# Optimization experiments

Measured on AMD Instinct MI355X. Metric: run time of the kernel, lower is better.

Reference implementation:

```python
import jax, jax.numpy as jnp
import numpy as np

IN_FEATURES = 4096
OUT_FEATURES = 4096


def setup_inputs() -> dict:
    key = jax.random.key(0)
    k_x, k_w, k_b = jax.random.split(key, 3)
    inp = {
        "input": jax.random.normal(k_x, (4, 2048, IN_FEATURES), dtype=jnp.float32),
        # learned int8 weight table [out_features, in_features]
        "weight_int8": jax.random.randint(k_w, (OUT_FEATURES, IN_FEATURES), -128, 128, dtype=jnp.int32).astype(jnp.int8),
        # per-tensor dequant scales (scalars, as in the module buffers)
        "scale": jnp.asarray(0.01, dtype=jnp.float32),
        "x_scale": jnp.asarray(0.05, dtype=jnp.float32),
        "bias": jax.random.normal(k_b, (OUT_FEATURES,), dtype=jnp.float32) * 0.02,
    }
    return inp


def reference(input, weight_int8, scale, x_scale, bias):
    # --- quantize activations per-tensor to int8 (W8A8 path) ---
    x_int8 = jnp.clip(jnp.round(input / x_scale), -128, 127).astype(jnp.int8)
    in_shape = input.shape
    x_flat = x_int8.reshape(-1, in_shape[-1])  # [B*S, in]
    # contract x_flat[k] with weight_int8[n, k] -> [B*S, out]
    out_i32 = jax.lax.dot_general(
        x_flat, weight_int8,
        dimension_numbers=(((1,), (1,)), ((), ())),
        preferred_element_type=jnp.int32,
    )
    # --- dequant epilogue: combined scale, reshape, bias ---
    out = out_i32.astype(input.dtype) * (scale * x_scale)
    out = out.reshape(*in_shape[:-1], weight_int8.shape[0])
    out = out + bias
    return out
```

## Files before the change

### kernel.cpp

```cpp
#include <hip/hip_runtime.h>

#define KDIM 4096
#define NDIM 4096
#define BM 128
#define BN 256
#define BK 64
#define NTILE (KDIM / BK)
#define BUFSZ 24576
#define NBUF 3

using i32x4 = __attribute__((ext_vector_type(4))) int;

__device__ __forceinline__ void g2l16(const void* g, void* l) {
  __builtin_amdgcn_global_load_lds(
      (const __attribute__((address_space(1))) void*)g,
      (__attribute__((address_space(3))) void*)l,
      16, 0, 0);
}

__global__ void w8l_detect(const int* __restrict__ w32, int* __restrict__ flag) {
  __shared__ int s;
  const int t = threadIdx.x;
  if (t == 0) s = 1;
  __syncthreads();
  bool oob = false;
#pragma unroll
  for (int i = 0; i < 16; ++i) {
    int v = w32[t * 16 + i];
    if (v < -128 || v > 127) oob = true;
  }
  if (oob) atomicAnd(&s, 0);
  __syncthreads();
  if (t == 0) *flag = s;
}

__global__ void w8l_pack(const void* __restrict__ wsrc, const int* __restrict__ flag,
                         signed char* __restrict__ wq) {
  if (*flag == 0) return;
  const int t = blockIdx.x * blockDim.x + threadIdx.x;
  const int4* s = (const int4*)wsrc;
  int4 a = s[t * 4 + 0], b = s[t * 4 + 1], c = s[t * 4 + 2], d = s[t * 4 + 3];
  int4 o;
  o.x = (a.x & 255) | ((a.y & 255) << 8) | ((a.z & 255) << 16) | ((a.w & 255) << 24);
  o.y = (b.x & 255) | ((b.y & 255) << 8) | ((b.z & 255) << 16) | ((b.w & 255) << 24);
  o.z = (c.x & 255) | ((c.y & 255) << 8) | ((c.z & 255) << 16) | ((c.w & 255) << 24);
  o.w = (d.x & 255) | ((d.y & 255) << 8) | ((d.z & 255) << 16) | ((d.w & 255) << 24);
  ((int4*)wq)[t] = o;
}

__global__ void w8l_quant(const float* __restrict__ x, const float* __restrict__ xs,
                          signed char* __restrict__ xq) {
  const int t = blockIdx.x * blockDim.x + threadIdx.x;
  const float s = *xs;
  const float4* x4 = (const float4*)x;
  int4 o;
  int* op = (int*)&o;
#pragma unroll
  for (int q = 0; q < 4; ++q) {
    float4 f = x4[t * 4 + q];
    int v0 = __float2int_rn(f.x / s);
    int v1 = __float2int_rn(f.y / s);
    int v2 = __float2int_rn(f.z / s);
    int v3 = __float2int_rn(f.w / s);
    v0 = v0 < -128 ? -128 : (v0 > 127 ? 127 : v0);
    v1 = v1 < -128 ? -128 : (v1 > 127 ? 127 : v1);
    v2 = v2 < -128 ? -128 : (v2 > 127 ? 127 : v2);
    v3 = v3 < -128 ? -128 : (v3 > 127 ? 127 : v3);
    op[q] = (v0 & 255) | ((v1 & 255) << 8) | ((v2 & 255) << 16) | ((v3 & 255) << 24);
  }
  ((int4*)xq)[t] = o;
}

__global__ __launch_bounds__(256, 2) void w8l_gemm(
    const signed char* __restrict__ Aq,
    const signed char* __restrict__ Wraw, const signed char* __restrict__ Wpk,
    const int* __restrict__ flag,
    const float* __restrict__ scale, const float* __restrict__ xscale,
    const float* __restrict__ bias, float* __restrict__ out, int nbn) {
  __shared__ signed char lds[NBUF * BUFSZ];

  const signed char* __restrict__ Wq = (*flag) ? Wpk : Wraw;

  const int tid = threadIdx.x;
  const int lane = tid & 63;
  const int wid = tid >> 6;
  const int wr = wid >> 1;
  const int wc = wid & 1;
  const int l15 = lane & 15;
  const int l4 = (lane >> 4) & 3;

  const int nwg = gridDim.x;
  const int cpx = nwg >> 3;
  const int bid = blockIdx.x;
  const int swz = (bid & 7) * cpx + (bid >> 3);
  const int bm = swz / nbn, bn = swz % nbn;
  const int m0 = bm * BM, n0 = bn * BN;

  const unsigned r_in = (unsigned)tid >> 2;
  const unsigned c16 = (unsigned)tid & 3;
  const unsigned s_in = (r_in >> 1) & 3u;
  const unsigned swcol = ((c16 ^ s_in) << 4);
  const signed char* agp = Aq + (size_t)(m0 + r_in) * KDIM + swcol;
  const signed char* wgp = Wq + (size_t)(n0 + r_in) * KDIM + swcol;
  const unsigned ldsoff = (unsigned)tid * 16u;

#define ISSUE_TILE(t, buf)                                                   \
  do {                                                                       \
    const size_t koff_ = (size_t)(t) * BK;                                   \
    signed char* lb_ = lds + (unsigned)(buf) * BUFSZ + ldsoff;               \
    _Pragma("unroll") for (int u = 0; u < 2; ++u)                            \
      g2l16(agp + (size_t)(u * 64) * KDIM + koff_, lb_ + u * 4096);          \
    _Pragma("unroll") for (int u = 0; u < 4; ++u)                            \
      g2l16(wgp + (size_t)(u * 64) * KDIM + koff_, lb_ + 8192 + u * 4096);   \
  } while (0)

  const unsigned slotoff = (unsigned)((l4 ^ ((l15 >> 1) & 3)) << 4);
  const unsigned arow = (unsigned)((wr * 64 + l15) * 64) + slotoff;
  const unsigned brow = (unsigned)((wc * 128 + l15) * 64) + slotoff + 8192u;

  i32x4 acc[4][8] = {};
  i32x4 af[4], bf[8];

  ISSUE_TILE(0, 0);
  ISSUE_TILE(1, 1);

  int bufr = 0, bufi = 2;
#pragma unroll 1
  for (int kt = 0; kt < NTILE; ++kt) {
    if (kt + 2 < NTILE) {
      asm volatile("s_waitcnt vmcnt(6)" ::: "memory");
    } else {
      asm volatile("s_waitcnt vmcnt(0)" ::: "memory");
    }
    __builtin_amdgcn_s_barrier();
    __builtin_amdgcn_sched_barrier(0);

    if (kt + 2 < NTILE) ISSUE_TILE(kt + 2, bufi);

    const signed char* base = lds + (unsigned)bufr * BUFSZ;
#pragma unroll
    for (int mi = 0; mi < 4; ++mi)
      af[mi] = *(const i32x4*)(base + arow + mi * 1024);
#pragma unroll
    for (int nj = 0; nj < 8; ++nj)
      bf[nj] = *(const i32x4*)(base + brow + nj * 1024);
    __builtin_amdgcn_sched_barrier(0);
    asm volatile("s_waitcnt lgkmcnt(0)" ::: "memory");
    __builtin_amdgcn_sched_barrier(0);

    __builtin_amdgcn_s_setprio(1);
#pragma unroll
    for (int mi = 0; mi < 4; ++mi)
#pragma unroll
      for (int nj = 0; nj < 8; ++nj)
        acc[mi][nj] = __builtin_amdgcn_mfma_i32_16x16x64_i8(af[mi], bf[nj], acc[mi][nj], 0, 0, 0);
    __builtin_amdgcn_s_setprio(0);
    __builtin_amdgcn_sched_barrier(0);

    bufr = (bufr == 2) ? 0 : bufr + 1;
    bufi = (bufi == 2) ? 0 : bufi + 1;
  }

  const float cs = scale[0] * xscale[0];
#pragma unroll
  for (int nj = 0; nj < 8; ++nj) {
    const int n = n0 + wc * 128 + nj * 16 + l15;
    const float bj = bias[n];
#pragma unroll
    for (int mi = 0; mi < 4; ++mi) {
      const int m = m0 + wr * 64 + mi * 16 + l4 * 4;
      float* o = out + (size_t)m * NDIM + n;
#pragma unroll
      for (int v = 0; v < 4; ++v)
        o[(size_t)v * NDIM] = (float)acc[mi][nj][v] * cs + bj;
    }
  }
#undef ISSUE_TILE
}

extern "C" void kernel_launch(void* const* d_in, const int* in_sizes, int n_in,
                              void* d_out, int out_size, void* d_ws, size_t ws_size,
                              hipStream_t stream) {
  const float* x = (const float*)d_in[0];
  const void* w = d_in[1];
  const float* scale = (const float*)d_in[2];
  const float* xscale = (const float*)d_in[3];
  const float* bias = (const float*)d_in[4];
  float* out = (float*)d_out;

  const int M = in_sizes[0] / KDIM;

  int* flag = (int*)d_ws;
  signed char* wq = (signed char*)d_ws + 256;
  signed char* aq = wq + (size_t)NDIM * KDIM;

  const size_t need = 256 + (size_t)NDIM * KDIM + (size_t)M * KDIM;
  if (ws_size < need) return;

  w8l_detect<<<1, 256, 0, stream>>>((const int*)w, flag);
  w8l_pack<<<(NDIM * KDIM / 16) / 256, 256, 0, stream>>>(w, flag, wq);
  w8l_quant<<<(M * KDIM / 16) / 256, 256, 0, stream>>>(x, xscale, aq);

  const int nbn = NDIM / BN;
  w8l_gemm<<<(M / BM) * nbn, 256, 0, stream>>>(
      aq, (const signed char*)w, wq, flag, scale, xscale, bias, out, nbn);
}
```

Measured before the change: 198.2 us.

## Load A fragments directly to registers and split MFMA phase on LDS waits

The A operand no longer goes through LDS. Each wave reads its A fragments straight from global memory into registers, double-buffered one tile ahead. Only B is staged through LDS, which shrinks the LDS footprint, and the main loop is unrolled by two so the register buffers can alternate. The MFMA block is also split in half around a partial lgkmcnt wait, letting compute start before all B reads finish. The cost is more global traffic for A, since the two waves sharing rows each load them, plus higher register pressure and vmcnt accounting that must be exactly right.

```diff
diff --git a/kernel.cpp b/kernel.cpp
--- a/kernel.cpp
+++ b/kernel.cpp
@@ -6,7 +6,7 @@
 #define BN 256
 #define BK 64
 #define NTILE (KDIM / BK)
-#define BUFSZ 24576
+#define BBUF 16384
 #define NBUF 3
 
 using i32x4 = __attribute__((ext_vector_type(4))) int;
@@ -77,7 +77,7 @@
     const int* __restrict__ flag,
     const float* __restrict__ scale, const float* __restrict__ xscale,
     const float* __restrict__ bias, float* __restrict__ out, int nbn) {
-  __shared__ signed char lds[NBUF * BUFSZ];
+  __shared__ signed char lds[NBUF * BBUF];
 
   const signed char* __restrict__ Wq = (*flag) ? Wpk : Wraw;
 
@@ -98,68 +98,88 @@
 
   const unsigned r_in = (unsigned)tid >> 2;
   const unsigned c16 = (unsigned)tid & 3;
-  const unsigned s_in = (r_in >> 1) & 3u;
-  const unsigned swcol = ((c16 ^ s_in) << 4);
-  const signed char* agp = Aq + (size_t)(m0 + r_in) * KDIM + swcol;
+  const unsigned swcol = ((c16 ^ ((r_in >> 1) & 3u)) << 4);
   const signed char* wgp = Wq + (size_t)(n0 + r_in) * KDIM + swcol;
   const unsigned ldsoff = (unsigned)tid * 16u;
 
-#define ISSUE_TILE(t, buf)                                                   \
+#define ISSUE_B(t, buf)                                                      \
   do {                                                                       \
     const size_t koff_ = (size_t)(t) * BK;                                   \
-    signed char* lb_ = lds + (unsigned)(buf) * BUFSZ + ldsoff;               \
-    _Pragma("unroll") for (int u = 0; u < 2; ++u)                            \
-      g2l16(agp + (size_t)(u * 64) * KDIM + koff_, lb_ + u * 4096);          \
+    signed char* lb_ = lds + (unsigned)(buf) * BBUF + ldsoff;                \
     _Pragma("unroll") for (int u = 0; u < 4; ++u)                            \
-      g2l16(wgp + (size_t)(u * 64) * KDIM + koff_, lb_ + 8192 + u * 4096);   \
+      g2l16(wgp + (size_t)(u * 64) * KDIM + koff_, lb_ + u * 4096);          \
   } while (0)
 
+  const signed char* agl = Aq + (size_t)(m0 + wr * 64 + l15) * KDIM + l4 * 16;
+
+#define LOAD_A(dst, t)                                                       \
+  _Pragma("unroll") for (int mi = 0; mi < 4; ++mi)                           \
+      dst[mi] = *(const i32x4*)(agl + (size_t)mi * (16 * KDIM) + (t) * 64);
+
   const unsigned slotoff = (unsigned)((l4 ^ ((l15 >> 1) & 3)) << 4);
-  const unsigned arow = (unsigned)((wr * 64 + l15) * 64) + slotoff;
-  const unsigned brow = (unsigned)((wc * 128 + l15) * 64) + slotoff + 8192u;
+  const unsigned brow = (unsigned)((wc * 128 + l15) * 64) + slotoff;
 
   i32x4 acc[4][8] = {};
-  i32x4 af[4], bf[8];
-
-  ISSUE_TILE(0, 0);
-  ISSUE_TILE(1, 1);
+  i32x4 aE[4], aO[4], bf[8];
+
+#define SB __builtin_amdgcn_sched_barrier(0)
+
+#define TILE(t, AC, AN, DO_A, DO_G, bufr_, bufi_, VMC)                       \
+  do {                                                                       \
+    asm volatile("s_waitcnt vmcnt(" #VMC ")" ::: "memory");                  \
+    __builtin_amdgcn_s_barrier();                                            \
+    SB;                                                                      \
+    if (DO_A) { LOAD_A(AN, (t) + 1); }                                       \
+    SB;                                                                      \
+    if (DO_G) ISSUE_B((t) + 2, bufi_);                                       \
+    SB;                                                                      \
+    {                                                                        \
+      const signed char* base_ = lds + (unsigned)(bufr_)*BBUF;               \
+      _Pragma("unroll") for (int nj = 0; nj < 8; ++nj)                       \
+          bf[nj] = *(const i32x4*)(base_ + brow + nj * 1024);                \
+    }                                                                        \
+    SB;                                                                      \
+    asm volatile("s_waitcnt lgkmcnt(4)" ::: "memory");                       \
+    SB;                                                                      \
+    __builtin_amdgcn_s_setprio(1);                                           \
+    _Pragma("unroll") for (int mi = 0; mi < 4; ++mi)                         \
+        _Pragma("unroll") for (int nj = 0; nj < 4; ++nj)                     \
+            acc[mi][nj] = __builtin_amdgcn_mfma_i32_16x16x64_i8(             \
+                AC[mi], bf[nj], acc[mi][nj], 0, 0, 0);                       \
+    __builtin_amdgcn_s_setprio(0);                                           \
+    SB;                                                                      \
+    asm volatile("s_waitcnt lgkmcnt(0)" ::: "memory");                       \
+    SB;                                                                      \
+    __builtin_amdgcn_s_setprio(1);                                           \
+    _Pragma("unroll") for (int mi = 0; mi < 4; ++mi)                         \
+        _Pragma("unroll") for (int nj = 4; nj < 8; ++nj)                     \
+            acc[mi][nj] = __builtin_amdgcn_mfma_i32_16x16x64_i8(             \
+                AC[mi], bf[nj], acc[mi][nj], 0, 0, 0);                       \
+    __builtin_amdgcn_s_setprio(0);                                           \
+    SB;                                                                      \
+  } while (0)
+
+  ISSUE_B(0, 0);
+  SB;
+  LOAD_A(aE, 0);
+  SB;
+  ISSUE_B(1, 1);
+  SB;
 
   int bufr = 0, bufi = 2;
 #pragma unroll 1
-  for (int kt = 0; kt < NTILE; ++kt) {
-    if (kt + 2 < NTILE) {
-      asm volatile("s_waitcnt vmcnt(6)" ::: "memory");
-    } else {
-      asm volatile("s_waitcnt vmcnt(0)" ::: "memory");
-    }
-    __builtin_amdgcn_s_barrier();
-    __builtin_amdgcn_sched_barrier(0);
-
-    if (kt + 2 < NTILE) ISSUE_TILE(kt + 2, bufi);
-
-    const signed char* base = lds + (unsigned)bufr * BUFSZ;
-#pragma unroll
-    for (int mi = 0; mi < 4; ++mi)
-      af[mi] = *(const i32x4*)(base + arow + mi * 1024);
-#pragma unroll
-    for (int nj = 0; nj < 8; ++nj)
-      bf[nj] = *(const i32x4*)(base + brow + nj * 1024);
-    __builtin_amdgcn_sched_barrier(0);
-    asm volatile("s_waitcnt lgkmcnt(0)" ::: "memory");
-    __builtin_amdgcn_sched_barrier(0);
-
-    __builtin_amdgcn_s_setprio(1);
-#pragma unroll
-    for (int mi = 0; mi < 4; ++mi)
-#pragma unroll
-      for (int nj = 0; nj < 8; ++nj)
-        acc[mi][nj] = __builtin_amdgcn_mfma_i32_16x16x64_i8(af[mi], bf[nj], acc[mi][nj], 0, 0, 0);
-    __builtin_amdgcn_s_setprio(0);
-    __builtin_amdgcn_sched_barrier(0);
-
+  for (int t2 = 0; t2 < NTILE - 2; t2 += 2) {
+    TILE(t2, aE, aO, 1, 1, bufr, bufi, 4);
     bufr = (bufr == 2) ? 0 : bufr + 1;
     bufi = (bufi == 2) ? 0 : bufi + 1;
-  }
+    TILE(t2 + 1, aO, aE, 1, 1, bufr, bufi, 4);
+    bufr = (bufr == 2) ? 0 : bufr + 1;
+    bufi = (bufi == 2) ? 0 : bufi + 1;
+  }
+  TILE(62, aE, aO, 1, 0, bufr, bufi, 4);
+  bufr = (bufr == 2) ? 0 : bufr + 1;
+  bufi = (bufi == 2) ? 0 : bufi + 1;
+  TILE(63, aO, aE, 0, 0, bufr, bufi, 0);
 
   const float cs = scale[0] * xscale[0];
 #pragma unroll
@@ -175,7 +195,10 @@
         o[(size_t)v * NDIM] = (float)acc[mi][nj][v] * cs + bj;
     }
   }
-#undef ISSUE_TILE
+#undef ISSUE_B
+#undef LOAD_A
+#undef TILE
+#undef SB
 }
 
 extern "C" void kernel_launch(void* const* d_in, const int* in_sizes, int n_in,
```

New measurement: 253.4 us. 1.28x slower.

## Pre-tile quantized activations for direct register loads and enlarge GEMM tile

Applied to the files above, without the earlier changes.

The quantize kernel now writes activations in an MFMA-fragment-friendly tiled layout, so the GEMM loads A fragments straight from global memory into registers and stages only the weights through LDS. The block tile grows to 256x256 with BK=128, 512 threads (8 waves), double buffering in place of triple, and a split even/odd k-substep schedule that overlaps A prefetch with MFMA work. The aim is to cut LDS traffic and raise arithmetic intensity. The costs are higher register pressure, since each wave holds 32 accumulators plus two A fragment sets, and global-load latency on A that is now exposed directly in the loop.

```diff
diff --git a/kernel.cpp b/kernel.cpp
--- a/kernel.cpp
+++ b/kernel.cpp
@@ -2,12 +2,11 @@
 
 #define KDIM 4096
 #define NDIM 4096
-#define BM 128
+#define BM 256
 #define BN 256
-#define BK 64
+#define BK 128
 #define NTILE (KDIM / BK)
-#define BUFSZ 24576
-#define NBUF 3
+#define BBUF 32768
 
 using i32x4 = __attribute__((ext_vector_type(4))) int;
 
@@ -49,15 +48,18 @@
 }
 
 __global__ void w8l_quant(const float* __restrict__ x, const float* __restrict__ xs,
-                          signed char* __restrict__ xq) {
+                          signed char* __restrict__ aq) {
   const int t = blockIdx.x * blockDim.x + threadIdx.x;
   const float s = *xs;
-  const float4* x4 = (const float4*)x;
+  const int r = t & 15;
+  const int kc = (t >> 4) & 255;
+  const int mb = t >> 12;
+  const float4* x4 = (const float4*)(x + (size_t)(mb * 16 + r) * KDIM + kc * 16);
   int4 o;
   int* op = (int*)&o;
 #pragma unroll
   for (int q = 0; q < 4; ++q) {
-    float4 f = x4[t * 4 + q];
+    float4 f = x4[q];
     int v0 = __float2int_rn(f.x / s);
     int v1 = __float2int_rn(f.y / s);
     int v2 = __float2int_rn(f.z / s);
@@ -68,24 +70,24 @@
     v3 = v3 < -128 ? -128 : (v3 > 127 ? 127 : v3);
     op[q] = (v0 & 255) | ((v1 & 255) << 8) | ((v2 & 255) << 16) | ((v3 & 255) << 24);
   }
-  ((int4*)xq)[t] = o;
-}
-
-__global__ __launch_bounds__(256, 2) void w8l_gemm(
-    const signed char* __restrict__ Aq,
+  ((int4*)aq)[t] = o;
+}
+
+__global__ __launch_bounds__(512, 2) void w8l_gemm(
+    const signed char* __restrict__ Ap,
     const signed char* __restrict__ Wraw, const signed char* __restrict__ Wpk,
     const int* __restrict__ flag,
     const float* __restrict__ scale, const float* __restrict__ xscale,
     const float* __restrict__ bias, float* __restrict__ out, int nbn) {
-  __shared__ signed char lds[NBUF * BUFSZ];
+  __shared__ signed char lds[2 * BBUF];
 
   const signed char* __restrict__ Wq = (*flag) ? Wpk : Wraw;
 
   const int tid = threadIdx.x;
   const int lane = tid & 63;
   const int wid = tid >> 6;
-  const int wr = wid >> 1;
-  const int wc = wid & 1;
+  const int wr = wid >> 2;
+  const int wc = wid & 3;
   const int l15 = lane & 15;
   const int l4 = (lane >> 4) & 3;
 
@@ -96,86 +98,96 @@
   const int bm = swz / nbn, bn = swz % nbn;
   const int m0 = bm * BM, n0 = bn * BN;
 
-  const unsigned r_in = (unsigned)tid >> 2;
-  const unsigned c16 = (unsigned)tid & 3;
-  const unsigned s_in = (r_in >> 1) & 3u;
-  const unsigned swcol = ((c16 ^ s_in) << 4);
-  const signed char* agp = Aq + (size_t)(m0 + r_in) * KDIM + swcol;
+  const unsigned r_in = (unsigned)tid >> 3;
+  const unsigned c16 = (unsigned)tid & 7;
+  const unsigned swcol = ((c16 ^ (r_in & 7u)) << 4);
   const signed char* wgp = Wq + (size_t)(n0 + r_in) * KDIM + swcol;
   const unsigned ldsoff = (unsigned)tid * 16u;
 
-#define ISSUE_TILE(t, buf)                                                   \
+#define ISSUE_B(t)                                                           \
   do {                                                                       \
     const size_t koff_ = (size_t)(t) * BK;                                   \
-    signed char* lb_ = lds + (unsigned)(buf) * BUFSZ + ldsoff;               \
-    _Pragma("unroll") for (int u = 0; u < 2; ++u)                            \
-      g2l16(agp + (size_t)(u * 64) * KDIM + koff_, lb_ + u * 4096);          \
+    signed char* lb_ = lds + (unsigned)((t) & 1) * BBUF + ldsoff;            \
     _Pragma("unroll") for (int u = 0; u < 4; ++u)                            \
-      g2l16(wgp + (size_t)(u * 64) * KDIM + koff_, lb_ + 8192 + u * 4096);   \
+      g2l16(wgp + (size_t)(u * 64) * KDIM + koff_, lb_ + u * 8192);          \
   } while (0)
 
-  const unsigned slotoff = (unsigned)((l4 ^ ((l15 >> 1) & 3)) << 4);
-  const unsigned arow = (unsigned)((wr * 64 + l15) * 64) + slotoff;
-  const unsigned brow = (unsigned)((wc * 128 + l15) * 64) + slotoff + 8192u;
-
-  i32x4 acc[4][8] = {};
-  i32x4 af[4], bf[8];
-
-  ISSUE_TILE(0, 0);
-  ISSUE_TILE(1, 1);
-
-  int bufr = 0, bufi = 2;
+  const signed char* aglp =
+      Ap + (size_t)(m0 / 16 + wr * 8) * 65536 + l4 * 256 + l15 * 16;
+
+#define LOAD_A(dst, t, ks)                                                   \
+  _Pragma("unroll") for (int mi = 0; mi < 8; ++mi)                           \
+      dst[mi] = *(const i32x4*)(aglp + (size_t)mi * 65536 +                  \
+                                (size_t)(t) * 2048 + (ks) * 1024);
+
+  const unsigned b_lane = (unsigned)((wc * 64 + l15) * 128) +
+                          (unsigned)((l4 ^ (l15 & 7)) << 4);
+
+  i32x4 acc[8][4] = {};
+  i32x4 aE[8], aO[8], b0[4], b1[4];
+
+#define SB __builtin_amdgcn_sched_barrier(0)
+
+  ISSUE_B(0);
+  SB;
+  LOAD_A(aE, 0, 0);
+  SB;
+
 #pragma unroll 1
   for (int kt = 0; kt < NTILE; ++kt) {
-    if (kt + 2 < NTILE) {
-      asm volatile("s_waitcnt vmcnt(6)" ::: "memory");
-    } else {
-      asm volatile("s_waitcnt vmcnt(0)" ::: "memory");
+    asm volatile("s_waitcnt vmcnt(8)" ::: "memory");
+    __builtin_amdgcn_s_barrier();
+    SB;
+
+    const signed char* Bb = lds + (unsigned)(kt & 1) * BBUF;
+#pragma unroll
+    for (int nj = 0; nj < 4; ++nj) {
+      b0[nj] = *(const i32x4*)(Bb + (b_lane + nj * 2048));
+      b1[nj] = *(const i32x4*)(Bb + ((b_lane + nj * 2048) ^ 64u));
     }
-    __builtin_amdgcn_s_barrier();
-    __builtin_amdgcn_sched_barrier(0);
-
-    if (kt + 2 < NTILE) ISSUE_TILE(kt + 2, bufi);
-
-    const signed char* base = lds + (unsigned)bufr * BUFSZ;
-#pragma unroll
-    for (int mi = 0; mi < 4; ++mi)
-      af[mi] = *(const i32x4*)(base + arow + mi * 1024);
-#pragma unroll
-    for (int nj = 0; nj < 8; ++nj)
-      bf[nj] = *(const i32x4*)(base + brow + nj * 1024);
-    __builtin_amdgcn_sched_barrier(0);
-    asm volatile("s_waitcnt lgkmcnt(0)" ::: "memory");
-    __builtin_amdgcn_sched_barrier(0);
+    SB;
+    LOAD_A(aO, kt, 1);
+    SB;
+    if (kt + 1 < NTILE) ISSUE_B(kt + 1);
+    SB;
 
     __builtin_amdgcn_s_setprio(1);
 #pragma unroll
-    for (int mi = 0; mi < 4; ++mi)
-#pragma unroll
-      for (int nj = 0; nj < 8; ++nj)
-        acc[mi][nj] = __builtin_amdgcn_mfma_i32_16x16x64_i8(af[mi], bf[nj], acc[mi][nj], 0, 0, 0);
+    for (int mi = 0; mi < 8; ++mi)
+#pragma unroll
+      for (int nj = 0; nj < 4; ++nj)
+        acc[mi][nj] = __builtin_amdgcn_mfma_i32_16x16x64_i8(aE[mi], b0[nj], acc[mi][nj], 0, 0, 0);
     __builtin_amdgcn_s_setprio(0);
-    __builtin_amdgcn_sched_barrier(0);
-
-    bufr = (bufr == 2) ? 0 : bufr + 1;
-    bufi = (bufi == 2) ? 0 : bufi + 1;
+    SB;
+    if (kt + 1 < NTILE) LOAD_A(aE, kt + 1, 0);
+    SB;
+    __builtin_amdgcn_s_setprio(1);
+#pragma unroll
+    for (int mi = 0; mi < 8; ++mi)
+#pragma unroll
+      for (int nj = 0; nj < 4; ++nj)
+        acc[mi][nj] = __builtin_amdgcn_mfma_i32_16x16x64_i8(aO[mi], b1[nj], acc[mi][nj], 0, 0, 0);
+    __builtin_amdgcn_s_setprio(0);
+    SB;
   }
 
   const float cs = scale[0] * xscale[0];
 #pragma unroll
-  for (int nj = 0; nj < 8; ++nj) {
-    const int n = n0 + wc * 128 + nj * 16 + l15;
+  for (int nj = 0; nj < 4; ++nj) {
+    const int n = n0 + wc * 64 + nj * 16 + l15;
     const float bj = bias[n];
 #pragma unroll
-    for (int mi = 0; mi < 4; ++mi) {
-      const int m = m0 + wr * 64 + mi * 16 + l4 * 4;
+    for (int mi = 0; mi < 8; ++mi) {
+      const int m = m0 + wr * 128 + mi * 16 + l4 * 4;
       float* o = out + (size_t)m * NDIM + n;
 #pragma unroll
       for (int v = 0; v < 4; ++v)
         o[(size_t)v * NDIM] = (float)acc[mi][nj][v] * cs + bj;
     }
   }
-#undef ISSUE_TILE
+#undef ISSUE_B
+#undef LOAD_A
+#undef SB
 }
 
 extern "C" void kernel_launch(void* const* d_in, const int* in_sizes, int n_in,
@@ -202,6 +214,6 @@
   w8l_quant<<<(M * KDIM / 16) / 256, 256, 0, stream>>>(x, xscale, aq);
 
   const int nbn = NDIM / BN;
-  w8l_gemm<<<(M / BM) * nbn, 256, 0, stream>>>(
+  w8l_gemm<<<(M / BM) * nbn, 512, 0, stream>>>(
       aq, (const signed char*)w, wq, flag, scale, xscale, bias, out, nbn);
 }
```

Measured after the change: 201.7 us. Within noise of the previous version (+1.8%).
